# Optimization experiments

Measured on AMD Instinct MI355X. Metric: run time of the kernel, lower is better.

Reference implementation:

```python
import jax, jax.numpy as jnp
import numpy as np

INPUT_SIZE = 8
HIDDEN = 64


def setup_inputs() -> dict:
    key = jax.random.key(0)
    ks = jax.random.split(key, 7)
    B, T = 4096, 512
    s_ih = 1.0 / np.sqrt(HIDDEN)
    return {
        "input": jax.random.normal(ks[0], (B, T, INPUT_SIZE), dtype=jnp.float32),
        # PyTorch LSTM params: gate order i, f, g, o stacked along dim 0
        "W_ih": jax.random.uniform(ks[1], (4 * HIDDEN, INPUT_SIZE), minval=-s_ih, maxval=s_ih, dtype=jnp.float32),
        "W_hh": jax.random.uniform(ks[2], (4 * HIDDEN, HIDDEN), minval=-s_ih, maxval=s_ih, dtype=jnp.float32),
        "b_ih": jax.random.uniform(ks[3], (4 * HIDDEN,), minval=-s_ih, maxval=s_ih, dtype=jnp.float32),
        "b_hh": jax.random.uniform(ks[4], (4 * HIDDEN,), minval=-s_ih, maxval=s_ih, dtype=jnp.float32),
        "W_dense": jax.random.uniform(ks[5], (1, HIDDEN), minval=-s_ih, maxval=s_ih, dtype=jnp.float32),
        "b_dense": jax.random.uniform(ks[6], (1,), minval=-s_ih, maxval=s_ih, dtype=jnp.float32),
    }


def _lstm_seq(x, W_ih, W_hh, b_ih, b_hh):
    # x: [B, T, I] -> h_seq: [B, T, H]
    B = x.shape[0]
    # precompute input projections for all timesteps: [T, B, 4H]
    x_proj = jnp.einsum('bti,gi->tbg', x, W_ih) + (b_ih + b_hh)

    def step(carry, xp):
        h, c = carry
        gates = xp + h @ W_hh.T  # [B, 4H]
        i, f, g, o = jnp.split(gates, 4, axis=-1)
        i = jax.nn.sigmoid(i)
        f = jax.nn.sigmoid(f)
        g = jnp.tanh(g)
        o = jax.nn.sigmoid(o)
        c = f * c + i * g
        h = o * jnp.tanh(c)
        return (h, c), h

    h0 = jnp.zeros((B, HIDDEN), dtype=x.dtype)
    c0 = jnp.zeros((B, HIDDEN), dtype=x.dtype)
    _, h_seq = jax.lax.scan(step, (h0, c0), x_proj)  # [T, B, H]
    return jnp.transpose(h_seq, (1, 0, 2))  # [B, T, H]


def reference(input, W_ih, W_hh, b_ih, b_hh, W_dense, b_dense):
    h_t = _lstm_seq(input, W_ih, W_hh, b_ih, b_hh)  # [B, T, H]
    return h_t @ W_dense.T + b_dense  # [B, T, 1]
```

## Files before the change

### kernel.cpp

```cpp
#include <hip/hip_runtime.h>

#define T_SEQ 512
#define ISZ 8
#define HID 64
#define L2E 1.44269504088896340736f

typedef __bf16 bf16x8 __attribute__((ext_vector_type(8)));
typedef float  f32x4  __attribute__((ext_vector_type(4)));

__device__ __forceinline__ float exp2_hw(float x) {
    float r; asm("v_exp_f32 %0, %1" : "=v"(r) : "v"(x)); return r;
}
__device__ __forceinline__ unsigned cvt_pk_bf16(float a, float b) {
    unsigned r; asm("v_cvt_pk_bf16_f32 %0, %1, %2" : "=v"(r) : "v"(a), "v"(b)); return r;
}

__global__ __launch_bounds__(256, 2) void lstm_v10_kernel(
    const float* __restrict__ x,
    const float* __restrict__ W_ih,
    const float* __restrict__ W_hh,
    const float* __restrict__ b_ih,
    const float* __restrict__ b_hh,
    const float* __restrict__ W_dense,
    const float* __restrict__ b_dense,
    float* __restrict__ out)
{
    __shared__ __align__(16) __bf16 hpl[2][16 * 64];
    __shared__ __align__(16) __bf16 xs[2][160];
    __shared__ __align__(16) __bf16 xz[8];

    const int tid  = threadIdx.x;
    const int lane = tid & 63;
    const int w    = tid >> 6;
    const int q    = lane >> 4;
    const int sub  = lane & 15;
    const int br   = 2 * (sub >> 2) + (sub & 1);
    const bool isLo = (sub & 2) != 0;
    const long b0  = (long)blockIdx.x * 8;

    bf16x8 Bg[4][3];
    float biasg[4];
    #pragma unroll
    for (int g = 0; g < 4; ++g) {
        const int m = g * HID + 16 * w + sub;
        const float sc = (g == 2) ? (2.0f * L2E) : (-L2E);
        biasg[g] = (b_ih[m] + b_hh[m]) * sc;
        #pragma unroll
        for (int s = 0; s < 3; ++s) {
            #pragma unroll
            for (int e = 0; e < 8; ++e) {
                const int k = 32 * s + 8 * q + e;
                float v = 0.0f;
                if (k < HID)            v = W_hh[m * HID + k] * sc;
                else if (k < HID + ISZ) v = W_ih[m * ISZ + (k - HID)] * sc;
                Bg[g][s][e] = (__bf16)v;
            }
        }
    }
    f32x4 Cs[4];
    #pragma unroll
    for (int g = 0; g < 4; ++g) { Cs[g][0] = biasg[g]; Cs[g][1] = biasg[g]; Cs[g][2] = 0.f; Cs[g][3] = 0.f; }

    bf16x8 Bwd[2];
    #pragma unroll
    for (int s = 0; s < 2; ++s) {
        #pragma unroll
        for (int e = 0; e < 8; ++e) {
            const int k = 32 * s + 8 * q + e;
            const float wv = W_dense[k];
            const __bf16 whi = (__bf16)wv;
            float val = (sub == 0) ? (float)whi : (sub == 1) ? (wv - (float)whi) : 0.0f;
            Bwd[s][e] = (__bf16)val;
        }
    }

    for (int i = tid; i < 512; i += 256) ((float*)&hpl[1][0])[i] = 0.0f;
    if (tid < 4) ((float*)&xz[0])[tid] = 0.0f;

    const int  pr = lane >> 1, ph = lane & 1;
    const float* xbase = x + ((b0 + pr) * (long)T_SEQ) * ISZ + ph * 4;
    const int  xoffH = pr * 8 + ph * 4;
    const int  xoffL = 64 + xoffH;

#define XWRITE(XV, DST)                                                      \
    {                                                                        \
        unsigned h01 = cvt_pk_bf16(XV.x, XV.y);                              \
        unsigned h23 = cvt_pk_bf16(XV.z, XV.w);                              \
        float f0 = __uint_as_float(h01 << 16);                               \
        float f1 = __uint_as_float(h01 & 0xffff0000u);                       \
        float f2 = __uint_as_float(h23 << 16);                               \
        float f3 = __uint_as_float(h23 & 0xffff0000u);                       \
        unsigned l01 = cvt_pk_bf16(XV.x - f0, XV.y - f1);                    \
        unsigned l23 = cvt_pk_bf16(XV.z - f2, XV.w - f3);                    \
        uint2 hh2; hh2.x = h01; hh2.y = h23;                                 \
        uint2 ll2; ll2.x = l01; ll2.y = l23;                                 \
        *(uint2*)&(DST)[xoffH] = hh2;                                        \
        *(uint2*)&(DST)[xoffL] = ll2;                                        \
    }

    float4 xp0, xp1, xp2, xp3;
    if (w == 3 && lane < 16) {
        float4 xv0 = *(const float4*)xbase;
        XWRITE(xv0, &xs[0][0])
        xp1 = *(const float4*)(xbase + (long)1 * ISZ);
        xp2 = *(const float4*)(xbase + (long)2 * ISZ);
        xp3 = *(const float4*)(xbase + (long)3 * ISZ);
        xp0 = *(const float4*)(xbase + (long)4 * ISZ);
    }

    const __bf16* xrd0 = (q == 0) ? &xs[0][(isLo ? 64 : 0) + br * 8] : &xz[0];
    const __bf16* xrd1 = (q == 0) ? &xs[1][(isLo ? 64 : 0) + br * 8] : &xz[0];

    float c0 = 0.f, c1 = 0.f;
    const float bd  = b_dense[0];
    const f32x4 Z   = {0.f, 0.f, 0.f, 0.f};
    const int  swz  = (sub & 7) << 3;
    const int  jme  = 16 * w + sub;

    float s0[4], s1[4];
    s0[0]=s0[1]=s0[2]=s0[3]=0.f;
    s1[0]=s1[1]=s1[2]=s1[3]=0.f;

    __syncthreads();

#define MF(A, B, C) __builtin_amdgcn_mfma_f32_16x16x32_bf16(A, B, C, 0, 0, 0)

#define STEP(P, PB, XR, XW, XP)                                                      \
    {                                                                                \
        const int t = tb + P;                                                        \
             \
              \
        if (w == 3 && lane < 16) {                                                   \
            XWRITE(XP, &xs[XW][0])                                                   \
            const int tn = (t + 5 < T_SEQ) ? (t + 5) : (T_SEQ - 1);                  \
            XP = *(const float4*)(xbase + (long)tn * ISZ);                           \
        }                                                                            \
            \
        bf16x8 Ax  = *(const bf16x8*)(XR);                                           \
        bf16x8 Ah0 = *(const bf16x8*)&hpl[PB][sub * 64 + ((8 * q)      ^ swz)];      \
        bf16x8 Ah1 = *(const bf16x8*)&hpl[PB][sub * 64 + ((32 + 8 * q) ^ swz)];      \
                                            \
        __builtin_amdgcn_s_setprio(1);                                               \
        f32x4 a0 = MF(Ax, Bg[0][2], Cs[0]);                                          \
        f32x4 a1 = MF(Ax, Bg[1][2], Cs[1]);                                          \
        f32x4 a2 = MF(Ax, Bg[2][2], Cs[2]);                                          \
        f32x4 a3 = MF(Ax, Bg[3][2], Cs[3]);                                          \
        a0 = MF(Ah0, Bg[0][0], a0); a0 = MF(Ah1, Bg[0][1], a0);                      \
        a1 = MF(Ah0, Bg[1][0], a1); a1 = MF(Ah1, Bg[1][1], a1);                      \
        a2 = MF(Ah0, Bg[2][0], a2); a2 = MF(Ah1, Bg[2][1], a2);                      \
        a3 = MF(Ah0, Bg[3][0], a3); a3 = MF(Ah1, Bg[3][1], a3);                      \
        __builtin_amdgcn_s_setprio(0);                                               \
                                 \
        if (w == 0) {                                                                \
            f32x4 oz = MF(Ah0, Bwd[0], Z);                                           \
            oz = MF(Ah1, Bwd[1], oz);                                                \
            float v0 = oz[0] + oz[2];                                                \
            float v1 = oz[1] + oz[3];                                                \
            v0 += __shfl_xor(v0, 1);                                                 \
            v1 += __shfl_xor(v1, 1);                                                 \
            s0[(P + 3) & 3] = v0;                                                    \
            s1[(P + 3) & 3] = v1;                                                    \
        }                                                                            \
                   \
        _Pragma("unroll")                                                            \
        for (int i = 0; i < 2; ++i) {                                                \
            const float gi = a0[i] + a0[2 + i];                                      \
            const float gf = a1[i] + a1[2 + i];                                      \
            const float gg = a2[i] + a2[2 + i];                                      \
            const float go = a3[i] + a3[2 + i];                                      \
            const float eA = exp2_hw(gi);                                            \
            const float eF = exp2_hw(gf);                                            \
            const float eB = exp2_hw(gg);                                            \
            const float ig = (eB - 1.0f) *                                           \
                __builtin_amdgcn_rcpf((1.0f + eA) * (1.0f + eB));                    \
            const float ff = __builtin_amdgcn_rcpf(1.0f + eF);                       \
            float cc = i ? c1 : c0;                                                  \
            cc = fmaf(ff, cc, ig);                                                   \
            if (i) c1 = cc; else c0 = cc;                                            \
            const float eO = exp2_hw(go);                                            \
            const float eC = exp2_hw(fminf(cc * (2.0f * L2E), 80.0f));               \
            const float hh = (eC - 1.0f) *                                           \
                __builtin_amdgcn_rcpf((1.0f + eO) * (1.0f + eC));                    \
            const __bf16 hi = (__bf16)hh;                                            \
            const __bf16 lo = (__bf16)(hh - (float)hi);                              \
            const int rh = 4 * q + i;                                                \
            const int rl = rh + 2;                                                   \
            hpl[PB ^ 1][rh * 64 + (jme ^ ((rh & 7) << 3))] = hi;                     \
            hpl[PB ^ 1][rl * 64 + (jme ^ ((rl & 7) << 3))] = lo;                     \
        }                                                                            \
                 \
        if (P == 0) {                                                                \
            if (w == 0 && sub == 0 && tb >= 4) {                                     \
                *(float4*)&out[(b0 + 2 * q) * T_SEQ + tb - 4] =                      \
                    make_float4(s0[0] + bd, s0[1] + bd, s0[2] + bd, s0[3] + bd);     \
                *(float4*)&out[(b0 + 2 * q + 1) * T_SEQ + tb - 4] =                  \
                    make_float4(s1[0] + bd, s1[1] + bd, s1[2] + bd, s1[3] + bd);     \
            }                                                                        \
        }                                                                            \
            \
        asm volatile("s_waitcnt lgkmcnt(0)" ::: "memory");                           \
        __builtin_amdgcn_s_barrier();                                                \
        __builtin_amdgcn_sched_barrier(0);                                           \
    }

    for (int tb = 0; tb < T_SEQ; tb += 4) {
        STEP(0, 1, xrd0, 1, xp1)
        STEP(1, 0, xrd1, 0, xp2)
        STEP(2, 1, xrd0, 1, xp3)
        STEP(3, 0, xrd1, 0, xp0)
    }
#undef STEP

    if (w == 0) {
        bf16x8 Eh0 = *(const bf16x8*)&hpl[1][sub * 64 + ((8 * q)      ^ swz)];
        bf16x8 Eh1 = *(const bf16x8*)&hpl[1][sub * 64 + ((32 + 8 * q) ^ swz)];
        f32x4 oz = MF(Eh0, Bwd[0], Z);
        oz = MF(Eh1, Bwd[1], oz);
        float v0 = oz[0] + oz[2];
        float v1 = oz[1] + oz[3];
        v0 += __shfl_xor(v0, 1);
        v1 += __shfl_xor(v1, 1);
        s0[3] = v0;
        s1[3] = v1;
        if (sub == 0) {
            *(float4*)&out[(b0 + 2 * q) * T_SEQ + (T_SEQ - 4)] =
                make_float4(s0[0] + bd, s0[1] + bd, s0[2] + bd, s0[3] + bd);
            *(float4*)&out[(b0 + 2 * q + 1) * T_SEQ + (T_SEQ - 4)] =
                make_float4(s1[0] + bd, s1[1] + bd, s1[2] + bd, s1[3] + bd);
        }
    }
#undef MF
#undef XWRITE
}

extern "C" void kernel_launch(void* const* d_in, const int* in_sizes, int n_in,
                              void* d_out, int out_size, void* d_ws, size_t ws_size,
                              hipStream_t stream) {
    const float* x       = (const float*)d_in[0];
    const float* W_ih    = (const float*)d_in[1];
    const float* W_hh    = (const float*)d_in[2];
    const float* b_ih    = (const float*)d_in[3];
    const float* b_hh    = (const float*)d_in[4];
    const float* W_dense = (const float*)d_in[5];
    const float* b_dense = (const float*)d_in[6];
    float* out = (float*)d_out;

    const int B = in_sizes[0] / (T_SEQ * ISZ);
    const int blocks = B / 8;
    lstm_v10_kernel<<<blocks, 256, 0, stream>>>(x, W_ih, W_hh, b_ih, b_hh,
                                                W_dense, b_dense, out);
}
```

Baseline: 275.3 us.

## Software-pipeline input projection MFMAs one step ahead and split recurrent chains

The input-projection MFMAs for step t+1 are now computed during step t and carried as accumulators, so the recurrent critical path only contains the h·W_hh MFMAs. The two K-halves of the recurrent product are accumulated into independent chains and summed with vector adds, which shortens the dependent MFMA chain. The x staging pipeline is deepened by one step (prefetch t+6, double-buffered xs preloaded for two steps). In exchange it uses more accumulator registers, which could pressure occupancy at 2 waves/SIMD, and adds extra VALU adds.

```diff
diff --git a/kernel.cpp b/kernel.cpp
--- a/kernel.cpp
+++ b/kernel.cpp
@@ -15,7 +15,7 @@
     unsigned r; asm("v_cvt_pk_bf16_f32 %0, %1, %2" : "=v"(r) : "v"(a), "v"(b)); return r;
 }
 
-__global__ __launch_bounds__(256, 2) void lstm_v10_kernel(
+__global__ __launch_bounds__(256, 2) void lstm_v12_kernel(
     const float* __restrict__ x,
     const float* __restrict__ W_ih,
     const float* __restrict__ W_hh,
@@ -98,14 +98,18 @@
         *(uint2*)&(DST)[xoffL] = ll2;                                        \
     }
 
-    float4 xp0, xp1, xp2, xp3;
+#define MF(A, B, C) __builtin_amdgcn_mfma_f32_16x16x32_bf16(A, B, C, 0, 0, 0)
+
+    float4 xpA, xpB, xpC, xpD;
     if (w == 3 && lane < 16) {
         float4 xv0 = *(const float4*)xbase;
         XWRITE(xv0, &xs[0][0])
-        xp1 = *(const float4*)(xbase + (long)1 * ISZ);
-        xp2 = *(const float4*)(xbase + (long)2 * ISZ);
-        xp3 = *(const float4*)(xbase + (long)3 * ISZ);
-        xp0 = *(const float4*)(xbase + (long)4 * ISZ);
+        float4 xv1 = *(const float4*)(xbase + (long)1 * ISZ);
+        XWRITE(xv1, &xs[1][0])
+        xpA = *(const float4*)(xbase + (long)2 * ISZ);
+        xpB = *(const float4*)(xbase + (long)3 * ISZ);
+        xpC = *(const float4*)(xbase + (long)4 * ISZ);
+        xpD = *(const float4*)(xbase + (long)5 * ISZ);
     }
 
     const __bf16* xrd0 = (q == 0) ? &xs[0][(isLo ? 64 : 0) + br * 8] : &xz[0];
@@ -123,32 +127,44 @@
 
     __syncthreads();
 
-#define MF(A, B, C) __builtin_amdgcn_mfma_f32_16x16x32_bf16(A, B, C, 0, 0, 0)
-
-#define STEP(P, PB, XR, XW, XP)                                                      \
+    f32x4 ax0, ax1, ax2, ax3;
+    {
+        bf16x8 Ax0 = *(const bf16x8*)xrd0;
+        ax0 = MF(Ax0, Bg[0][2], Cs[0]);
+        ax1 = MF(Ax0, Bg[1][2], Cs[1]);
+        ax2 = MF(Ax0, Bg[2][2], Cs[2]);
+        ax3 = MF(Ax0, Bg[3][2], Cs[3]);
+    }
+    __syncthreads();
+
+#define STEP(P, PB, XRN, XW, XP)                                                     \
     {                                                                                \
         const int t = tb + P;                                                        \
              \
-              \
         if (w == 3 && lane < 16) {                                                   \
             XWRITE(XP, &xs[XW][0])                                                   \
-            const int tn = (t + 5 < T_SEQ) ? (t + 5) : (T_SEQ - 1);                  \
+            const int tn = (t + 6 < T_SEQ) ? (t + 6) : (T_SEQ - 1);                  \
             XP = *(const float4*)(xbase + (long)tn * ISZ);                           \
         }                                                                            \
-            \
-        bf16x8 Ax  = *(const bf16x8*)(XR);                                           \
+              \
+        bf16x8 Axn = *(const bf16x8*)(XRN);                                          \
         bf16x8 Ah0 = *(const bf16x8*)&hpl[PB][sub * 64 + ((8 * q)      ^ swz)];      \
         bf16x8 Ah1 = *(const bf16x8*)&hpl[PB][sub * 64 + ((32 + 8 * q) ^ swz)];      \
-                                            \
+               \
+               \
         __builtin_amdgcn_s_setprio(1);                                               \
-        f32x4 a0 = MF(Ax, Bg[0][2], Cs[0]);                                          \
-        f32x4 a1 = MF(Ax, Bg[1][2], Cs[1]);                                          \
-        f32x4 a2 = MF(Ax, Bg[2][2], Cs[2]);                                          \
-        f32x4 a3 = MF(Ax, Bg[3][2], Cs[3]);                                          \
-        a0 = MF(Ah0, Bg[0][0], a0); a0 = MF(Ah1, Bg[0][1], a0);                      \
-        a1 = MF(Ah0, Bg[1][0], a1); a1 = MF(Ah1, Bg[1][1], a1);                      \
-        a2 = MF(Ah0, Bg[2][0], a2); a2 = MF(Ah1, Bg[2][1], a2);                      \
-        a3 = MF(Ah0, Bg[3][0], a3); a3 = MF(Ah1, Bg[3][1], a3);                      \
+        f32x4 p0 = MF(Ah0, Bg[0][0], ax0);                                           \
+        f32x4 p1 = MF(Ah0, Bg[1][0], ax1);                                           \
+        f32x4 p2 = MF(Ah0, Bg[2][0], ax2);                                           \
+        f32x4 p3 = MF(Ah0, Bg[3][0], ax3);                                           \
+        f32x4 r0 = MF(Ah1, Bg[0][1], Z);                                             \
+        f32x4 r1 = MF(Ah1, Bg[1][1], Z);                                             \
+        f32x4 r2 = MF(Ah1, Bg[2][1], Z);                                             \
+        f32x4 r3 = MF(Ah1, Bg[3][1], Z);                                             \
+        ax0 = MF(Axn, Bg[0][2], Cs[0]);                                              \
+        ax1 = MF(Axn, Bg[1][2], Cs[1]);                                              \
+        ax2 = MF(Axn, Bg[2][2], Cs[2]);                                              \
+        ax3 = MF(Axn, Bg[3][2], Cs[3]);                                              \
         __builtin_amdgcn_s_setprio(0);                                               \
                                  \
         if (w == 0) {                                                                \
@@ -161,7 +177,11 @@
             s0[(P + 3) & 3] = v0;                                                    \
             s1[(P + 3) & 3] = v1;                                                    \
         }                                                                            \
-                   \
+               \
+        f32x4 a0 = p0 + r0;                                                          \
+        f32x4 a1 = p1 + r1;                                                          \
+        f32x4 a2 = p2 + r2;                                                          \
+        f32x4 a3 = p3 + r3;                                                          \
         _Pragma("unroll")                                                            \
         for (int i = 0; i < 2; ++i) {                                                \
             const float gi = a0[i] + a0[2 + i];                                      \
@@ -204,10 +224,10 @@
     }
 
     for (int tb = 0; tb < T_SEQ; tb += 4) {
-        STEP(0, 1, xrd0, 1, xp1)
-        STEP(1, 0, xrd1, 0, xp2)
-        STEP(2, 1, xrd0, 1, xp3)
-        STEP(3, 0, xrd1, 0, xp0)
+        STEP(0, 1, xrd1, 0, xpA)
+        STEP(1, 0, xrd0, 1, xpB)
+        STEP(2, 1, xrd1, 0, xpC)
+        STEP(3, 0, xrd0, 1, xpD)
     }
 #undef STEP
 
@@ -247,6 +267,6 @@
 
     const int B = in_sizes[0] / (T_SEQ * ISZ);
     const int blocks = B / 8;
-    lstm_v10_kernel<<<blocks, 256, 0, stream>>>(x, W_ih, W_hh, b_ih, b_hh,
+    lstm_v12_kernel<<<blocks, 256, 0, stream>>>(x, W_ih, W_hh, b_ih, b_hh,
                                                 W_dense, b_dense, out);
 }
```

Result: slower. 310.0 us (+12.6%).

## Ping-pong two batch groups per block to overlap MFMA and activation phases

Applied to the files above, without the earlier changes.

Each block now holds two independent 8-sequence groups in 512 threads, and the per-step work is split into an MFMA phase and an activation phase. The two groups are staggered so that one group's matrix multiplies run while the other group's transcendental activations run, with a barrier between half-slots. This aims to hide the serial MFMA→activation dependency of the recurrence by interleaving two independent chains. In exchange it doubles the number of block-wide barriers per timestep and halves the number of blocks, which drops occupancy from two blocks per CU to one.

```diff
diff --git a/kernel.cpp b/kernel.cpp
--- a/kernel.cpp
+++ b/kernel.cpp
@@ -15,7 +15,7 @@
     unsigned r; asm("v_cvt_pk_bf16_f32 %0, %1, %2" : "=v"(r) : "v"(a), "v"(b)); return r;
 }
 
-__global__ __launch_bounds__(256, 2) void lstm_v10_kernel(
+__global__ __launch_bounds__(512, 1) void lstm_v13_kernel(
     const float* __restrict__ x,
     const float* __restrict__ W_ih,
     const float* __restrict__ W_hh,
@@ -25,24 +25,29 @@
     const float* __restrict__ b_dense,
     float* __restrict__ out)
 {
-    __shared__ __align__(16) __bf16 hpl[2][16 * 64];
-    __shared__ __align__(16) __bf16 xs[2][160];
+    __shared__ __align__(16) __bf16 hpl[2][2][16 * 64];
+    __shared__ __align__(16) __bf16 xs[2][2][160];
     __shared__ __align__(16) __bf16 xz[8];
 
     const int tid  = threadIdx.x;
     const int lane = tid & 63;
     const int w    = tid >> 6;
+    const int grp  = w >> 2;
+    const int wg   = w & 3;
     const int q    = lane >> 4;
     const int sub  = lane & 15;
     const int br   = 2 * (sub >> 2) + (sub & 1);
     const bool isLo = (sub & 2) != 0;
-    const long b0  = (long)blockIdx.x * 8;
+    const long b0  = (long)blockIdx.x * 16 + grp * 8;
+
+    __bf16 (*hplG)[16 * 64] = hpl[grp];
+    __bf16 (*xsG)[160]      = xs[grp];
 
     bf16x8 Bg[4][3];
     float biasg[4];
     #pragma unroll
     for (int g = 0; g < 4; ++g) {
-        const int m = g * HID + 16 * w + sub;
+        const int m = g * HID + 16 * wg + sub;
         const float sc = (g == 2) ? (2.0f * L2E) : (-L2E);
         biasg[g] = (b_ih[m] + b_hh[m]) * sc;
         #pragma unroll
@@ -74,7 +79,8 @@
         }
     }
 
-    for (int i = tid; i < 512; i += 256) ((float*)&hpl[1][0])[i] = 0.0f;
+    ((float*)&hpl[0][1][0])[tid] = 0.0f;
+    ((float*)&hpl[1][1][0])[tid] = 0.0f;
     if (tid < 4) ((float*)&xz[0])[tid] = 0.0f;
 
     const int  pr = lane >> 1, ph = lane & 1;
@@ -99,59 +105,56 @@
     }
 
     float4 xp0, xp1, xp2, xp3;
-    if (w == 3 && lane < 16) {
+    if (wg == 3 && lane < 16) {
         float4 xv0 = *(const float4*)xbase;
-        XWRITE(xv0, &xs[0][0])
+        XWRITE(xv0, &xsG[0][0])
         xp1 = *(const float4*)(xbase + (long)1 * ISZ);
         xp2 = *(const float4*)(xbase + (long)2 * ISZ);
         xp3 = *(const float4*)(xbase + (long)3 * ISZ);
         xp0 = *(const float4*)(xbase + (long)4 * ISZ);
     }
 
-    const __bf16* xrd0 = (q == 0) ? &xs[0][(isLo ? 64 : 0) + br * 8] : &xz[0];
-    const __bf16* xrd1 = (q == 0) ? &xs[1][(isLo ? 64 : 0) + br * 8] : &xz[0];
+    const __bf16* xrd0 = (q == 0) ? &xsG[0][(isLo ? 64 : 0) + br * 8] : &xz[0];
+    const __bf16* xrd1 = (q == 0) ? &xsG[1][(isLo ? 64 : 0) + br * 8] : &xz[0];
 
     float c0 = 0.f, c1 = 0.f;
     const float bd  = b_dense[0];
     const f32x4 Z   = {0.f, 0.f, 0.f, 0.f};
     const int  swz  = (sub & 7) << 3;
-    const int  jme  = 16 * w + sub;
+    const int  jme  = 16 * wg + sub;
 
     float s0[4], s1[4];
     s0[0]=s0[1]=s0[2]=s0[3]=0.f;
     s1[0]=s1[1]=s1[2]=s1[3]=0.f;
 
+    f32x4 a0 = Z, a1 = Z, a2 = Z, a3 = Z;
+
     __syncthreads();
 
 #define MF(A, B, C) __builtin_amdgcn_mfma_f32_16x16x32_bf16(A, B, C, 0, 0, 0)
 
-#define STEP(P, PB, XR, XW, XP)                                                      \
+#define MFMA_PH(P, XR, XP)                                                           \
     {                                                                                \
         const int t = tb + P;                                                        \
-             \
-              \
-        if (w == 3 && lane < 16) {                                                   \
-            XWRITE(XP, &xs[XW][0])                                                   \
+        if (wg == 3 && lane < 16) {                                                  \
+            XWRITE(XP, &xsG[(P + 1) & 1][0])                                         \
             const int tn = (t + 5 < T_SEQ) ? (t + 5) : (T_SEQ - 1);                  \
             XP = *(const float4*)(xbase + (long)tn * ISZ);                           \
         }                                                                            \
-            \
         bf16x8 Ax  = *(const bf16x8*)(XR);                                           \
-        bf16x8 Ah0 = *(const bf16x8*)&hpl[PB][sub * 64 + ((8 * q)      ^ swz)];      \
-        bf16x8 Ah1 = *(const bf16x8*)&hpl[PB][sub * 64 + ((32 + 8 * q) ^ swz)];      \
-                                            \
+        bf16x8 Ah0 = *(const bf16x8*)&hplG[(P + 1) & 1][sub * 64 + ((8 * q)      ^ swz)]; \
+        bf16x8 Ah1 = *(const bf16x8*)&hplG[(P + 1) & 1][sub * 64 + ((32 + 8 * q) ^ swz)]; \
         __builtin_amdgcn_s_setprio(1);                                               \
-        f32x4 a0 = MF(Ax, Bg[0][2], Cs[0]);                                          \
-        f32x4 a1 = MF(Ax, Bg[1][2], Cs[1]);                                          \
-        f32x4 a2 = MF(Ax, Bg[2][2], Cs[2]);                                          \
-        f32x4 a3 = MF(Ax, Bg[3][2], Cs[3]);                                          \
+        a0 = MF(Ax, Bg[0][2], Cs[0]);                                                \
+        a1 = MF(Ax, Bg[1][2], Cs[1]);                                                \
+        a2 = MF(Ax, Bg[2][2], Cs[2]);                                                \
+        a3 = MF(Ax, Bg[3][2], Cs[3]);                                                \
         a0 = MF(Ah0, Bg[0][0], a0); a0 = MF(Ah1, Bg[0][1], a0);                      \
         a1 = MF(Ah0, Bg[1][0], a1); a1 = MF(Ah1, Bg[1][1], a1);                      \
         a2 = MF(Ah0, Bg[2][0], a2); a2 = MF(Ah1, Bg[2][1], a2);                      \
         a3 = MF(Ah0, Bg[3][0], a3); a3 = MF(Ah1, Bg[3][1], a3);                      \
         __builtin_amdgcn_s_setprio(0);                                               \
-                                 \
-        if (w == 0) {                                                                \
+        if (wg == 0) {                                                               \
             f32x4 oz = MF(Ah0, Bwd[0], Z);                                           \
             oz = MF(Ah1, Bwd[1], oz);                                                \
             float v0 = oz[0] + oz[2];                                                \
@@ -160,8 +163,17 @@
             v1 += __shfl_xor(v1, 1);                                                 \
             s0[(P + 3) & 3] = v0;                                                    \
             s1[(P + 3) & 3] = v1;                                                    \
+            if (P == 0 && sub == 0 && tb >= 4) {                                     \
+                *(float4*)&out[(b0 + 2 * q) * T_SEQ + tb - 4] =                      \
+                    make_float4(s0[0] + bd, s0[1] + bd, s0[2] + bd, s0[3] + bd);     \
+                *(float4*)&out[(b0 + 2 * q + 1) * T_SEQ + tb - 4] =                  \
+                    make_float4(s1[0] + bd, s1[1] + bd, s1[2] + bd, s1[3] + bd);     \
+            }                                                                        \
         }                                                                            \
-                   \
+    }
+
+#define ACT_PH(HWPL)                                                                 \
+    {                                                                                \
         _Pragma("unroll")                                                            \
         for (int i = 0; i < 2; ++i) {                                                \
             const float gi = a0[i] + a0[2 + i];                                      \
@@ -185,35 +197,37 @@
             const __bf16 lo = (__bf16)(hh - (float)hi);                              \
             const int rh = 4 * q + i;                                                \
             const int rl = rh + 2;                                                   \
-            hpl[PB ^ 1][rh * 64 + (jme ^ ((rh & 7) << 3))] = hi;                     \
-            hpl[PB ^ 1][rl * 64 + (jme ^ ((rl & 7) << 3))] = lo;                     \
+            hplG[HWPL][rh * 64 + (jme ^ ((rh & 7) << 3))] = hi;                      \
+            hplG[HWPL][rl * 64 + (jme ^ ((rl & 7) << 3))] = lo;                      \
         }                                                                            \
-                 \
-        if (P == 0) {                                                                \
-            if (w == 0 && sub == 0 && tb >= 4) {                                     \
-                *(float4*)&out[(b0 + 2 * q) * T_SEQ + tb - 4] =                      \
-                    make_float4(s0[0] + bd, s0[1] + bd, s0[2] + bd, s0[3] + bd);     \
-                *(float4*)&out[(b0 + 2 * q + 1) * T_SEQ + tb - 4] =                  \
-                    make_float4(s1[0] + bd, s1[1] + bd, s1[2] + bd, s1[3] + bd);     \
-            }                                                                        \
-        }                                                                            \
-            \
-        asm volatile("s_waitcnt lgkmcnt(0)" ::: "memory");                           \
-        __builtin_amdgcn_s_barrier();                                                \
-        __builtin_amdgcn_sched_barrier(0);                                           \
-    }
+    }
+
+#define BARRIER()                                                                    \
+    asm volatile("s_waitcnt lgkmcnt(0)" ::: "memory");                               \
+    __builtin_amdgcn_s_barrier();                                                    \
+    __builtin_amdgcn_sched_barrier(0);
+
+#define SLOT(P, XR, XPREG)                                                           \
+    if (grp == 0) { MFMA_PH(P, XR, XPREG) }                                          \
+    else { if ((tb + P) != 0) { ACT_PH(((P + 1) & 1)) } }                            \
+    BARRIER()                                                                        \
+    if (grp == 0) { ACT_PH((P & 1)) }                                                \
+    else { MFMA_PH(P, XR, XPREG) }                                                   \
+    BARRIER()
 
     for (int tb = 0; tb < T_SEQ; tb += 4) {
-        STEP(0, 1, xrd0, 1, xp1)
-        STEP(1, 0, xrd1, 0, xp2)
-        STEP(2, 1, xrd0, 1, xp3)
-        STEP(3, 0, xrd1, 0, xp0)
-    }
-#undef STEP
-
-    if (w == 0) {
-        bf16x8 Eh0 = *(const bf16x8*)&hpl[1][sub * 64 + ((8 * q)      ^ swz)];
-        bf16x8 Eh1 = *(const bf16x8*)&hpl[1][sub * 64 + ((32 + 8 * q) ^ swz)];
+        SLOT(0, xrd0, xp1)
+        SLOT(1, xrd1, xp2)
+        SLOT(2, xrd0, xp3)
+        SLOT(3, xrd1, xp0)
+    }
+#undef SLOT
+
+    if (grp == 1) { ACT_PH(1) }
+    __syncthreads();
+    if (wg == 0) {
+        bf16x8 Eh0 = *(const bf16x8*)&hplG[1][sub * 64 + ((8 * q)      ^ swz)];
+        bf16x8 Eh1 = *(const bf16x8*)&hplG[1][sub * 64 + ((32 + 8 * q) ^ swz)];
         f32x4 oz = MF(Eh0, Bwd[0], Z);
         oz = MF(Eh1, Bwd[1], oz);
         float v0 = oz[0] + oz[2];
@@ -230,6 +244,9 @@
         }
     }
 #undef MF
+#undef MFMA_PH
+#undef ACT_PH
+#undef BARRIER
 #undef XWRITE
 }
 
@@ -246,7 +263,7 @@
     float* out = (float*)d_out;
 
     const int B = in_sizes[0] / (T_SEQ * ISZ);
-    const int blocks = B / 8;
-    lstm_v10_kernel<<<blocks, 256, 0, stream>>>(x, W_ih, W_hh, b_ih, b_hh,
+    const int blocks = B / 16;
+    lstm_v13_kernel<<<blocks, 512, 0, stream>>>(x, W_ih, W_hh, b_ih, b_hh,
                                                 W_dense, b_dense, out);
 }
```

After: 369.5 us. 34.2% more time.
